# Optimization experiments

Measured on AMD Instinct MI355X. Metric: run time of the kernel, lower is better.

## Reference

```python
import jax, jax.numpy as jnp
import numpy as np

DIM = 1024
HEADS = 16
DIM_HEAD = 64


def setup_inputs() -> dict:
    key = jax.random.key(0)
    k1, k2 = jax.random.split(key)
    x = jax.random.normal(k1, (2, 2048, DIM), dtype=jnp.float32)
    # to_qkv: Linear(dim, 3*heads*dim_head, bias=False); torch weight is [out,in],
    # we store the transposed [in,out] form for x @ W.
    W_qkv = jax.random.normal(k2, (DIM, 3 * HEADS * DIM_HEAD), dtype=jnp.float32) * (DIM ** -0.5)
    return {"x": x, "W_qkv": W_qkv}


def reference(x, W_qkv):
    b, n, _ = x.shape
    h, d = HEADS, DIM_HEAD
    scale = d ** -0.5
    qkv = x @ W_qkv                              # [b, n, 3*h*d]
    q, k, v = jnp.split(qkv, 3, axis=-1)
    # 'b n (h d) -> b h n d'
    q = q.reshape(b, n, h, d).transpose(0, 2, 1, 3)
    k = k.reshape(b, n, h, d).transpose(0, 2, 1, 3)
    v = v.reshape(b, n, h, d).transpose(0, 2, 1, 3)
    dots = jnp.einsum('bhnd,bhmd->bhnm', q, k) * scale
    attn = jax.nn.softmax(dots, axis=-1)
    out = jnp.einsum('bhnm,bhmd->bhnd', attn, v)
    out = out.transpose(0, 2, 1, 3).reshape(b, n, h * d)  # 'b h n d -> b n (h d)'
    return out + x  # residual (to_out is never applied in the source forward)
```

## Files before the change

### kernel.cpp

```cpp
#include <hip/hip_runtime.h>

#define DIM   1024
#define NQKV  3072
#define SEQ   2048
#define HEADS 16
#define DHEAD 64
#define M_TOT 4096

typedef __bf16 bf16;
typedef __bf16 bf16x8 __attribute__((ext_vector_type(8)));
typedef float  f32x4  __attribute__((ext_vector_type(4)));

typedef const __attribute__((address_space(1))) unsigned int gu32;
typedef __attribute__((address_space(3))) unsigned int su32;

static __device__ __forceinline__ unsigned short f2b(float f) {
    bf16 h = (bf16)f;
    return __builtin_bit_cast(unsigned short, h);
}

#define CAST_BLOCKS (M_TOT * DIM / (256 * 4))
#define TR_NB (NQKV / 64)
__global__ void prep_kernel(const float* __restrict__ x,
                            unsigned short* __restrict__ xb,
                            const float* __restrict__ W,
                            unsigned short* __restrict__ Wt) {
    __shared__ float tile[64][65];
    const int id  = blockIdx.x;
    const int tid = threadIdx.x;
    if (id < CAST_BLOCKS) {
        int i = (id * 256 + tid) * 4;
        float4 v = *(const float4*)(x + i);
        ushort4 o;
        o.x = f2b(v.x); o.y = f2b(v.y); o.z = f2b(v.z); o.w = f2b(v.w);
        *(ushort4*)(xb + i) = o;
    } else {
        int t  = id - CAST_BLOCKS;
        int nb = t % TR_NB;
        int kb = t / TR_NB;
        #pragma unroll
        for (int p = 0; p < 4; p++) {
            int kl = p * 16 + (tid >> 4);
            int nl = (tid & 15) * 4;
            float4 v = *(const float4*)&W[(size_t)(kb * 64 + kl) * NQKV + nb * 64 + nl];
            tile[nl + 0][kl] = v.x;
            tile[nl + 1][kl] = v.y;
            tile[nl + 2][kl] = v.z;
            tile[nl + 3][kl] = v.w;
        }
        __syncthreads();
        #pragma unroll
        for (int p = 0; p < 2; p++) {
            int nl = p * 32 + (tid >> 3);
            int k8 = (tid & 7) * 8;
            int n  = nb * 64 + nl;
            float s = (n < 1024) ? 0.18033688f : 1.0f;
            float4 a = *(const float4*)&tile[nl][k8];
            float4 b = *(const float4*)&tile[nl][k8 + 4];
            ushort4 o0, o1;
            o0.x = f2b(a.x * s); o0.y = f2b(a.y * s); o0.z = f2b(a.z * s); o0.w = f2b(a.w * s);
            o1.x = f2b(b.x * s); o1.y = f2b(b.y * s); o1.z = f2b(b.z * s); o1.w = f2b(b.w * s);
            uint4 pk;
            pk.x = ((unsigned)o0.y << 16) | o0.x;
            pk.y = ((unsigned)o0.w << 16) | o0.z;
            pk.z = ((unsigned)o1.y << 16) | o1.x;
            pk.w = ((unsigned)o1.w << 16) | o1.z;
            *(uint4*)&Wt[(size_t)n * DIM + kb * 64 + k8] = pk;
        }
    }
}

#define LDC 136
__global__ __launch_bounds__(256) void qkv_gemm_kernel(
    const unsigned short* __restrict__ A,
    const unsigned short* __restrict__ Bt,
    unsigned short* __restrict__ Qw,
    unsigned short* __restrict__ Kw,
    unsigned short* __restrict__ Vtw)
{
    __shared__ __align__(16) unsigned char smem[128 * LDC * 2];
    unsigned short* As = (unsigned short*)smem;
    unsigned short* Bs = (unsigned short*)(smem + 16384);
    unsigned short* Cs = (unsigned short*)smem;

    const int tid  = threadIdx.x;
    const int m0   = blockIdx.y * 128;
    const int n0   = blockIdx.x * 128;
    const int w    = tid >> 6;
    const int lane = tid & 63;
    const int l16  = lane & 15;
    const int quad = lane >> 4;
    const int wm   = (w >> 1) * 64;
    const int wn   = (w & 1) * 64;
    const int srow = lane >> 3;
    const int scol = (lane & 7) * 8;

    f32x4 acc[4][4];
    const f32x4 fzero = {0.f, 0.f, 0.f, 0.f};
    for (int i = 0; i < 4; i++)
        for (int j = 0; j < 4; j++) acc[i][j] = fzero;

    const unsigned short* Ag = A  + (size_t)(m0 + w * 32 + srow) * DIM + scol;
    const unsigned short* Bg = Bt + (size_t)(n0 + w * 32 + srow) * DIM + scol;

    for (int kt = 0; kt < DIM; kt += 64) {
        #pragma unroll
        for (int j = 0; j < 4; j++) {
            __builtin_amdgcn_global_load_lds((gu32*)(Ag + kt + (size_t)j * 8 * DIM),
                                             (su32*)&As[(w * 32 + j * 8) * 64], 16, 0, 0);
            __builtin_amdgcn_global_load_lds((gu32*)(Bg + kt + (size_t)j * 8 * DIM),
                                             (su32*)&Bs[(w * 32 + j * 8) * 64], 16, 0, 0);
        }
        __syncthreads();
        #pragma unroll
        for (int s = 0; s < 2; s++) {
            bf16x8 af[4], bfr[4];
            #pragma unroll
            for (int i = 0; i < 4; i++) {
                af[i]  = *(const bf16x8*)(&As[(wm + i * 16 + l16) * 64 + s * 32 + quad * 8]);
                bfr[i] = *(const bf16x8*)(&Bs[(wn + i * 16 + l16) * 64 + s * 32 + quad * 8]);
            }
            #pragma unroll
            for (int i = 0; i < 4; i++)
                #pragma unroll
                for (int j = 0; j < 4; j++)
                    acc[i][j] = __builtin_amdgcn_mfma_f32_16x16x32_bf16(af[i], bfr[j], acc[i][j], 0, 0, 0);
        }
        __syncthreads();
    }

    const int part = n0 >> 10;
    const int h0   = (n0 & 1023) >> 6;
    const int b    = m0 >> 11;
    const int np0  = m0 & 2047;

    if (part < 2) {
        #pragma unroll
        for (int i = 0; i < 4; i++)
            #pragma unroll
            for (int j = 0; j < 4; j++)
                #pragma unroll
                for (int r = 0; r < 4; r++)
                    Cs[(wm + i * 16 + quad * 4 + r) * LDC + wn + j * 16 + l16] = f2b(acc[i][j][r]);
        __syncthreads();
        unsigned short* dst = (part == 0) ? Qw : Kw;
        #pragma unroll
        for (int pass = 0; pass < 8; pass++) {
            int mi = pass * 16 + (tid >> 4);
            int ci = (tid & 15) * 8;
            uint4 v = *(const uint4*)&Cs[mi * LDC + ci];
            int bh = b * HEADS + h0 + (ci >> 6);
            *(uint4*)&dst[((size_t)bh * SEQ + np0 + mi) * DHEAD + (ci & 63)] = v;
        }
    } else {
        #pragma unroll
        for (int i = 0; i < 4; i++)
            #pragma unroll
            for (int j = 0; j < 4; j++) {
                ushort4 pk;
                pk.x = f2b(acc[i][j][0]); pk.y = f2b(acc[i][j][1]);
                pk.z = f2b(acc[i][j][2]); pk.w = f2b(acc[i][j][3]);
                *(ushort4*)&Cs[(wn + j * 16 + l16) * LDC + wm + i * 16 + quad * 4] = pk;
            }
        __syncthreads();
        #pragma unroll
        for (int pass = 0; pass < 8; pass++) {
            int ci = pass * 16 + (tid >> 4);
            int mi = (tid & 15) * 8;
            uint4 v = *(const uint4*)&Cs[ci * LDC + mi];
            int bh = b * HEADS + h0 + (ci >> 6);
            *(uint4*)&Vtw[((size_t)bh * DHEAD + (ci & 63)) * SEQ + np0 + mi] = v;
        }
    }
}

#define LDK 72
__global__ __launch_bounds__(256) void attn_kernel(
    const unsigned short* __restrict__ Qw,
    const unsigned short* __restrict__ Kw,
    const unsigned short* __restrict__ Vtw,
    const float* __restrict__ x,
    float* __restrict__ out)
{
    __shared__ __align__(16) unsigned short Ks[2][64 * LDK];
    __shared__ __align__(16) unsigned short Vs[2][64 * LDK];
    const int id  = blockIdx.x;
    const int qt  = id >> 5;
    const int bh  = ((id & 7) << 2) | ((id >> 3) & 3);
    const int tid = threadIdx.x;
    const int w   = tid >> 6, lane = tid & 63;
    const int l16 = lane & 15, quad = lane >> 4;

    const unsigned short* Qbase = Qw + ((size_t)bh * SEQ + qt * 64 + w * 16 + l16) * DHEAD;
    bf16x8 qf[2];
    qf[0] = *(const bf16x8*)(Qbase + quad * 8);
    qf[1] = *(const bf16x8*)(Qbase + 32 + quad * 8);

    bf16x8 ones;
    #pragma unroll
    for (int j = 0; j < 8; j++) ones[j] = (bf16)1.0f;

    f32x4 o[4], dsum;
    const f32x4 fzero = {0.f, 0.f, 0.f, 0.f};
    #pragma unroll
    for (int d = 0; d < 4; d++) o[d] = fzero;
    dsum = fzero;

    const unsigned short* Kg = Kw  + (size_t)bh * SEQ * DHEAD;
    const unsigned short* Vg = Vtw + (size_t)bh * DHEAD * SEQ;

    const int r0 = tid >> 3, c0 = (tid & 7) * 8;
    const int pr0 = ((r0 >> 2) & 1) * 16 + ((r0 >> 3) & 3) * 4 + (r0 & 3);

    uint4 kreg0 = *(const uint4*)(Kg + (size_t)r0 * DHEAD + c0);
    uint4 kreg1 = *(const uint4*)(Kg + (size_t)(r0 + 32) * DHEAD + c0);
    uint4 vreg0 = *(const uint4*)(Vg + (size_t)r0 * SEQ + c0);
    uint4 vreg1 = *(const uint4*)(Vg + (size_t)(r0 + 32) * SEQ + c0);
    *(uint4*)&Ks[0][pr0 * LDK + c0]        = kreg0;
    *(uint4*)&Ks[0][(pr0 + 32) * LDK + c0] = kreg1;
    *(uint4*)&Vs[0][r0 * LDK + c0]         = vreg0;
    *(uint4*)&Vs[0][(r0 + 32) * LDK + c0]  = vreg1;
    kreg0 = *(const uint4*)(Kg + (size_t)(64 + r0) * DHEAD + c0);
    kreg1 = *(const uint4*)(Kg + (size_t)(64 + r0 + 32) * DHEAD + c0);
    vreg0 = *(const uint4*)(Vg + (size_t)r0 * SEQ + 64 + c0);
    vreg1 = *(const uint4*)(Vg + (size_t)(r0 + 32) * SEQ + 64 + c0);

    for (int t = 0; t < SEQ / 64; t++) {
        const int cur = t & 1, nxt = cur ^ 1;
        __syncthreads();
        *(uint4*)&Ks[nxt][pr0 * LDK + c0]        = kreg0;
        *(uint4*)&Ks[nxt][(pr0 + 32) * LDK + c0] = kreg1;
        *(uint4*)&Vs[nxt][r0 * LDK + c0]         = vreg0;
        *(uint4*)&Vs[nxt][(r0 + 32) * LDK + c0]  = vreg1;
        int kvn = ((t + 2) & (SEQ / 64 - 1)) * 64;
        kreg0 = *(const uint4*)(Kg + (size_t)(kvn + r0) * DHEAD + c0);
        kreg1 = *(const uint4*)(Kg + (size_t)(kvn + r0 + 32) * DHEAD + c0);
        vreg0 = *(const uint4*)(Vg + (size_t)r0 * SEQ + kvn + c0);
        vreg1 = *(const uint4*)(Vg + (size_t)(r0 + 32) * SEQ + kvn + c0);

        f32x4 sacc[4];
        #pragma unroll
        for (int ki = 0; ki < 4; ki++) sacc[ki] = fzero;
        #pragma unroll
        for (int s = 0; s < 2; s++)
            #pragma unroll
            for (int ki = 0; ki < 4; ki++) {
                bf16x8 kf = *(const bf16x8*)(
                    &Ks[cur][(ki * 16 + l16) * LDK + s * 32 + quad * 8]);
                sacc[ki] = __builtin_amdgcn_mfma_f32_16x16x32_bf16(kf, qf[s], sacc[ki], 0, 0, 0);
            }

        bf16x8 pf[2];
        #pragma unroll
        for (int s = 0; s < 2; s++)
            #pragma unroll
            for (int half = 0; half < 2; half++) {
                int ki = 2 * s + half;
                #pragma unroll
                for (int r = 0; r < 4; r++)
                    pf[s][half * 4 + r] = (bf16)__builtin_amdgcn_exp2f(sacc[ki][r]);
            }

        #pragma unroll
        for (int s = 0; s < 2; s++) {
            dsum = __builtin_amdgcn_mfma_f32_16x16x32_bf16(pf[s], ones, dsum, 0, 0, 0);
            #pragma unroll
            for (int d = 0; d < 4; d++) {
                bf16x8 vf = *(const bf16x8*)(&Vs[cur][(d * 16 + l16) * LDK + s * 32 + quad * 8]);
                o[d] = __builtin_amdgcn_mfma_f32_16x16x32_bf16(pf[s], vf, o[d], 0, 0, 0);
            }
        }
    }

    float lr[4];
    #pragma unroll
    for (int r = 0; r < 4; r++) lr[r] = __builtin_amdgcn_rcpf(dsum[r]);

    const int b = bh >> 4, h = bh & 15;
    #pragma unroll
    for (int di = 0; di < 4; di++)
        #pragma unroll
        for (int r = 0; r < 4; r++) {
            int np  = qt * 64 + w * 16 + quad * 4 + r;
            int col = h * 64 + di * 16 + l16;
            size_t g = ((size_t)(b * SEQ + np)) * DIM + col;
            out[g] = o[di][r] * lr[r] + x[g];
        }
}

extern "C" void kernel_launch(void* const* d_in, const int* in_sizes, int n_in,
                              void* d_out, int out_size, void* d_ws, size_t ws_size,
                              hipStream_t stream) {
    const float* x  = (const float*)d_in[0];
    const float* Wq = (const float*)d_in[1];
    float* out = (float*)d_out;

    unsigned short* xb = (unsigned short*)d_ws;
    unsigned short* Wt = xb + (size_t)M_TOT * DIM;
    unsigned short* Qw = Wt + (size_t)NQKV * DIM;
    unsigned short* Kw = Qw + (size_t)32 * SEQ * DHEAD;
    unsigned short* Vt = Kw + (size_t)32 * SEQ * DHEAD;

    prep_kernel<<<CAST_BLOCKS + TR_NB * (DIM / 64), 256, 0, stream>>>(x, xb, Wq, Wt);
    qkv_gemm_kernel<<<dim3(NQKV / 128, M_TOT / 128), 256, 0, stream>>>(xb, Wt, Qw, Kw, Vt);
    attn_kernel<<<(SEQ / 64) * 32, 256, 0, stream>>>(Qw, Kw, Vt, x, out);
}
```

Baseline: 177.5 us.

## Process 128 query rows per attention block to reuse K/V tiles

Each wave now handles two 16-row query sub-tiles instead of one, so every block covers 128 queries and the grid is halved. Each K/V fragment loaded from shared memory feeds twice as many MFMAs, which halves global and LDS K/V traffic per query. In exchange register pressure roughly doubles for the accumulators, and the grid drops to 512 blocks, which may lower occupancy and parallelism on the GPU.

Result: faster. 172.9 us (-2.6%).

```diff
diff --git a/kernel.cpp b/kernel.cpp
--- a/kernel.cpp
+++ b/kernel.cpp
@@ -191,20 +191,26 @@
     const int w   = tid >> 6, lane = tid & 63;
     const int l16 = lane & 15, quad = lane >> 4;
 
-    const unsigned short* Qbase = Qw + ((size_t)bh * SEQ + qt * 64 + w * 16 + l16) * DHEAD;
-    bf16x8 qf[2];
-    qf[0] = *(const bf16x8*)(Qbase + quad * 8);
-    qf[1] = *(const bf16x8*)(Qbase + 32 + quad * 8);
+    const unsigned short* Qb = Qw + ((size_t)bh * SEQ + qt * 128 + w * 32 + l16) * DHEAD;
+    bf16x8 qf[2][2];
+    #pragma unroll
+    for (int qh = 0; qh < 2; qh++) {
+        qf[qh][0] = *(const bf16x8*)(Qb + qh * 16 * DHEAD + quad * 8);
+        qf[qh][1] = *(const bf16x8*)(Qb + qh * 16 * DHEAD + 32 + quad * 8);
+    }
 
     bf16x8 ones;
     #pragma unroll
     for (int j = 0; j < 8; j++) ones[j] = (bf16)1.0f;
 
-    f32x4 o[4], dsum;
+    f32x4 o[2][4], dsum[2];
     const f32x4 fzero = {0.f, 0.f, 0.f, 0.f};
     #pragma unroll
-    for (int d = 0; d < 4; d++) o[d] = fzero;
-    dsum = fzero;
+    for (int qh = 0; qh < 2; qh++) {
+        #pragma unroll
+        for (int d = 0; d < 4; d++) o[qh][d] = fzero;
+        dsum[qh] = fzero;
+    }
 
     const unsigned short* Kg = Kw  + (size_t)bh * SEQ * DHEAD;
     const unsigned short* Vg = Vtw + (size_t)bh * DHEAD * SEQ;
@@ -238,54 +244,63 @@
         vreg0 = *(const uint4*)(Vg + (size_t)r0 * SEQ + kvn + c0);
         vreg1 = *(const uint4*)(Vg + (size_t)(r0 + 32) * SEQ + kvn + c0);
 
-        f32x4 sacc[4];
-        #pragma unroll
-        for (int ki = 0; ki < 4; ki++) sacc[ki] = fzero;
+        f32x4 sacc[2][4];
+        #pragma unroll
+        for (int qh = 0; qh < 2; qh++)
+            #pragma unroll
+            for (int ki = 0; ki < 4; ki++) sacc[qh][ki] = fzero;
         #pragma unroll
         for (int s = 0; s < 2; s++)
             #pragma unroll
             for (int ki = 0; ki < 4; ki++) {
                 bf16x8 kf = *(const bf16x8*)(
                     &Ks[cur][(ki * 16 + l16) * LDK + s * 32 + quad * 8]);
-                sacc[ki] = __builtin_amdgcn_mfma_f32_16x16x32_bf16(kf, qf[s], sacc[ki], 0, 0, 0);
-            }
-
-        bf16x8 pf[2];
-        #pragma unroll
-        for (int s = 0; s < 2; s++)
-            #pragma unroll
-            for (int half = 0; half < 2; half++) {
-                int ki = 2 * s + half;
+                sacc[0][ki] = __builtin_amdgcn_mfma_f32_16x16x32_bf16(kf, qf[0][s], sacc[0][ki], 0, 0, 0);
+                sacc[1][ki] = __builtin_amdgcn_mfma_f32_16x16x32_bf16(kf, qf[1][s], sacc[1][ki], 0, 0, 0);
+            }
+
+        bf16x8 pf[2][2];
+        #pragma unroll
+        for (int qh = 0; qh < 2; qh++)
+            #pragma unroll
+            for (int s = 0; s < 2; s++)
                 #pragma unroll
-                for (int r = 0; r < 4; r++)
-                    pf[s][half * 4 + r] = (bf16)__builtin_amdgcn_exp2f(sacc[ki][r]);
-            }
+                for (int half = 0; half < 2; half++) {
+                    int ki = 2 * s + half;
+                    #pragma unroll
+                    for (int r = 0; r < 4; r++)
+                        pf[qh][s][half * 4 + r] = (bf16)__builtin_amdgcn_exp2f(sacc[qh][ki][r]);
+                }
 
         #pragma unroll
         for (int s = 0; s < 2; s++) {
-            dsum = __builtin_amdgcn_mfma_f32_16x16x32_bf16(pf[s], ones, dsum, 0, 0, 0);
+            dsum[0] = __builtin_amdgcn_mfma_f32_16x16x32_bf16(pf[0][s], ones, dsum[0], 0, 0, 0);
+            dsum[1] = __builtin_amdgcn_mfma_f32_16x16x32_bf16(pf[1][s], ones, dsum[1], 0, 0, 0);
             #pragma unroll
             for (int d = 0; d < 4; d++) {
                 bf16x8 vf = *(const bf16x8*)(&Vs[cur][(d * 16 + l16) * LDK + s * 32 + quad * 8]);
-                o[d] = __builtin_amdgcn_mfma_f32_16x16x32_bf16(pf[s], vf, o[d], 0, 0, 0);
-            }
-        }
-    }
-
-    float lr[4];
-    #pragma unroll
-    for (int r = 0; r < 4; r++) lr[r] = __builtin_amdgcn_rcpf(dsum[r]);
+                o[0][d] = __builtin_amdgcn_mfma_f32_16x16x32_bf16(pf[0][s], vf, o[0][d], 0, 0, 0);
+                o[1][d] = __builtin_amdgcn_mfma_f32_16x16x32_bf16(pf[1][s], vf, o[1][d], 0, 0, 0);
+            }
+        }
+    }
 
     const int b = bh >> 4, h = bh & 15;
     #pragma unroll
-    for (int di = 0; di < 4; di++)
-        #pragma unroll
-        for (int r = 0; r < 4; r++) {
-            int np  = qt * 64 + w * 16 + quad * 4 + r;
-            int col = h * 64 + di * 16 + l16;
-            size_t g = ((size_t)(b * SEQ + np)) * DIM + col;
-            out[g] = o[di][r] * lr[r] + x[g];
-        }
+    for (int qh = 0; qh < 2; qh++) {
+        float lr[4];
+        #pragma unroll
+        for (int r = 0; r < 4; r++) lr[r] = __builtin_amdgcn_rcpf(dsum[qh][r]);
+        #pragma unroll
+        for (int di = 0; di < 4; di++)
+            #pragma unroll
+            for (int r = 0; r < 4; r++) {
+                int np  = qt * 128 + w * 32 + qh * 16 + quad * 4 + r;
+                int col = h * 64 + di * 16 + l16;
+                size_t g = ((size_t)(b * SEQ + np)) * DIM + col;
+                out[g] = o[qh][di][r] * lr[r] + x[g];
+            }
+    }
 }
 
 extern "C" void kernel_launch(void* const* d_in, const int* in_sizes, int n_in,
@@ -303,5 +318,5 @@
 
     prep_kernel<<<CAST_BLOCKS + TR_NB * (DIM / 64), 256, 0, stream>>>(x, xb, Wq, Wt);
     qkv_gemm_kernel<<<dim3(NQKV / 128, M_TOT / 128), 256, 0, stream>>>(xb, Wt, Qw, Kw, Vt);
-    attn_kernel<<<(SEQ / 64) * 32, 256, 0, stream>>>(Qw, Kw, Vt, x, out);
-}
+    attn_kernel<<<(SEQ / 128) * 32, 256, 0, stream>>>(Qw, Kw, Vt, x, out);
+}
```
